# Optimization experiments

Hardware: AMD Instinct MI355X
Metric: run time of the kernel (lower is better)

## Reference

```python
import jax, jax.numpy as jnp
import numpy as np

B, D, H, W, N, R, K = 8, 192, 64, 64, 16, 6, 4
L = H * W
EPS = 1e-5


def setup_inputs() -> dict:
    key = jax.random.key(0)
    ks = jax.random.split(key, 6)
    return {
        "x": jax.random.normal(ks[0], (B, D, H, W), jnp.float32),
        "x_proj_weight": jax.random.normal(ks[1], (K, R + 2 * N, D), jnp.float32) * 0.05,
        "dt_projs_weight": jax.random.normal(ks[2], (K, D, R), jnp.float32) * 0.1,
        "dt_projs_bias": jax.random.normal(ks[3], (K, D), jnp.float32) * 0.1,
        "A_logs": jax.random.uniform(ks[4], (K * D, N), jnp.float32),  # A = -exp(A_logs) in (-e,-1)
        "Ds": jax.random.uniform(ks[5], (K * D,), jnp.float32),
        "norm_weight": jnp.ones((D,), jnp.float32),
        "norm_bias": jnp.zeros((D,), jnp.float32),
    }


def cross_scan(x):
    # x: [B,D,H,W] -> xs: [B,K=4,D,L]
    b, d, h, w = x.shape
    x0 = x.reshape(b, d, h * w)                      # row-major scan
    x1 = x.transpose(0, 1, 3, 2).reshape(b, d, h * w)  # column-major scan
    return jnp.stack([x0, x1, x0[..., ::-1], x1[..., ::-1]], axis=1)


def cross_merge(ys, h, w):
    # ys: [B,K=4,D,L] -> y: [B,D,L]
    b, k, d, l = ys.shape
    y01 = ys[:, 0] + ys[:, 2, :, ::-1]
    y23 = ys[:, 1] + ys[:, 3, :, ::-1]
    # undo the transpose of the column-major scan
    y23 = y23.reshape(b, d, w, h).transpose(0, 1, 3, 2).reshape(b, d, l)
    return y01 + y23


def selective_scan(u, dt, A, Bs, Cs, Dskip, dt_bias):
    # u, dt: [B,K,D,L]; A: [K,D,N]; Bs, Cs: [B,K,N,L]; Dskip, dt_bias: [K,D]
    dt = jax.nn.softplus(dt + dt_bias[None, :, :, None])
    dBu = dt * u
    # L-first for scan
    dt_l = dt.transpose(3, 0, 1, 2)    # [L,B,K,D]
    dBu_l = dBu.transpose(3, 0, 1, 2)  # [L,B,K,D]
    Bs_l = Bs.transpose(3, 0, 1, 2)    # [L,B,K,N]
    Cs_l = Cs.transpose(3, 0, 1, 2)    # [L,B,K,N]

    def step(h, inp):
        dt_t, dBu_t, B_t, C_t = inp
        dA = jnp.exp(dt_t[..., None] * A)                     # [B,K,D,N]
        h = h * dA + dBu_t[..., None] * B_t[:, :, None, :]    # [B,K,D,N]
        y = jnp.einsum('bkdn,bkn->bkd', h, C_t)
        return h, y

    h0 = jnp.zeros((u.shape[0], K, D, N), u.dtype)
    _, ys = jax.lax.scan(step, h0, (dt_l, dBu_l, Bs_l, Cs_l))
    ys = ys.transpose(1, 2, 3, 0)                             # [B,K,D,L]
    return ys + Dskip[None, :, :, None] * u


def reference(x, x_proj_weight, dt_projs_weight, dt_projs_bias, A_logs, Ds, norm_weight, norm_bias):
    b, d, h, w = x.shape
    l = h * w
    xs = cross_scan(x)                                        # [B,K,D,L]
    x_dbl = jnp.einsum('bkdl,kcd->bkcl', xs, x_proj_weight)   # [B,K,R+2N,L]
    dts, Bs, Cs = jnp.split(x_dbl, [R, R + N], axis=2)        # [B,K,R,L],[B,K,N,L],[B,K,N,L]
    dts = jnp.einsum('bkrl,kdr->bkdl', dts, dt_projs_weight)  # [B,K,D,L]
    A = -jnp.exp(A_logs).reshape(K, d, N)
    ys = selective_scan(xs, dts, A, Bs, Cs, Ds.reshape(K, d), dt_projs_bias)
    y = cross_merge(ys, h, w)                                 # [B,D,L]
    # out_norm (LayerNorm over channel dim, v0 path)
    y = y.transpose(0, 2, 1)                                  # [B,L,D]
    mu = jnp.mean(y, axis=-1, keepdims=True)
    var = jnp.mean(jnp.square(y - mu), axis=-1, keepdims=True)
    y = (y - mu) * jax.lax.rsqrt(var + EPS) * norm_weight + norm_bias
    return y.reshape(b, h, w, d).astype(x.dtype)
```

## Files before the change

kernel.cpp:

```cpp
#include <hip/hip_runtime.h>
#include <hip/hip_bf16.h>

#define LL 4096
#define DD 192
#define NN 16
#define NCH 128
#define LC  32

typedef float v2f __attribute__((ext_vector_type(2)));
typedef float f32x4 __attribute__((ext_vector_type(4)));
typedef short bf16x8 __attribute__((ext_vector_type(8)));

__device__ __forceinline__ v2f v2(float a, float b) { v2f r; r.x = a; r.y = b; return r; }
__device__ __forceinline__ float fexp2(float x) { return __builtin_amdgcn_exp2f(x); }

__global__ __launch_bounds__(192) void k_wprep(
    const float* __restrict__ Wp, __hip_bfloat16* __restrict__ Whi,
    __hip_bfloat16* __restrict__ Wlo)
{
  const int d = threadIdx.x;
  const int r = blockIdx.x;
  const int k = r / 48, cc = r % 48;
  float v = 0.f;
  if      (cc < 6)               v = Wp[((size_t)k * 38 + cc) * DD + d];
  else if (cc >= 8  && cc < 24)  v = Wp[((size_t)k * 38 + 6  + (cc - 8))  * DD + d];
  else if (cc >= 24 && cc < 40)  v = Wp[((size_t)k * 38 + 22 + (cc - 24)) * DD + d];
  const __hip_bfloat16 hi = __float2bfloat16(v);
  Whi[(size_t)r * DD + d] = hi;
  Wlo[(size_t)r * DD + d] = __float2bfloat16(v - __bfloat162float(hi));
}

__global__ __launch_bounds__(256) void k_an(
    const float* __restrict__ Alog, float* __restrict__ Ant)
{
  const int i = blockIdx.x * 256 + threadIdx.x;
  Ant[i] = -__expf(Alog[i]) * 1.4426950408889634f;
}

__global__ __launch_bounds__(256) void k_xt(
    const float* __restrict__ x, __hip_bfloat16* __restrict__ xh,
    __hip_bfloat16* __restrict__ xl)
{
  __shared__ float tile[64][65];
  const int b = blockIdx.z, d0 = blockIdx.y * 64, p0 = blockIdx.x * 64;
  const int tx = threadIdx.x & 63, ty = threadIdx.x >> 6;
#pragma unroll
  for (int r = ty; r < 64; r += 4)
    tile[r][tx] = x[((size_t)b * DD + d0 + r) * LL + p0 + tx];
  __syncthreads();
#pragma unroll
  for (int pr = ty; pr < 64; pr += 4) {
    const float vv = tile[tx][pr];
    const __hip_bfloat16 hi = __float2bfloat16(vv);
    const size_t idx = ((size_t)b * LL + p0 + pr) * DD + d0 + tx;
    xh[idx] = hi;
    xl[idx] = __float2bfloat16(vv - __bfloat162float(hi));
  }
}

__global__ __launch_bounds__(192) void k_mfproj(
    const __hip_bfloat16* __restrict__ xh, const __hip_bfloat16* __restrict__ xl,
    const __hip_bfloat16* __restrict__ Whi, const __hip_bfloat16* __restrict__ Wlo,
    float* __restrict__ dtr, float* __restrict__ Bsv, float* __restrict__ Csv)
{
  const int tid  = threadIdx.x;
  const int w    = tid >> 6;
  const int lane = tid & 63;
  const int n    = lane & 15;
  const int quad = lane >> 4;
  const int p0   = blockIdx.x * 16;
  const int b    = blockIdx.y;
  const int p    = p0 + n;

  const short* __restrict__ xhp = (const short*)xh + ((size_t)b * LL + p) * DD + quad * 8;
  const short* __restrict__ xlp = (const short*)xl + ((size_t)b * LL + p) * DD + quad * 8;
  const short* __restrict__ whp = (const short*)Whi + ((size_t)(w * 4) * 16 + n) * DD + quad * 8;
  const short* __restrict__ wlp = (const short*)Wlo + ((size_t)(w * 4) * 16 + n) * DD + quad * 8;

  f32x4 acc[4];
#pragma unroll
  for (int m = 0; m < 4; ++m) acc[m] = (f32x4){0.f, 0.f, 0.f, 0.f};

#pragma unroll
  for (int ks = 0; ks < 6; ++ks) {
    const bf16x8 bh = *(const bf16x8*)(xhp + ks * 32);
    const bf16x8 bl = *(const bf16x8*)(xlp + ks * 32);
#pragma unroll
    for (int m = 0; m < 4; ++m) {
      const bf16x8 ah = *(const bf16x8*)(whp + (size_t)m * 16 * DD + ks * 32);
      const bf16x8 al = *(const bf16x8*)(wlp + (size_t)m * 16 * DD + ks * 32);
      acc[m] = __builtin_amdgcn_mfma_f32_16x16x32_bf16(ah, bh, acc[m], 0, 0, 0);
      acc[m] = __builtin_amdgcn_mfma_f32_16x16x32_bf16(ah, bl, acc[m], 0, 0, 0);
      acc[m] = __builtin_amdgcn_mfma_f32_16x16x32_bf16(al, bh, acc[m], 0, 0, 0);
    }
  }

  const int sg = ((p & 63) << 6) | (p >> 6);
  int lsv[4] = { p, sg, LL - 1 - p, LL - 1 - sg };

#pragma unroll
  for (int m = 0; m < 4; ++m) {
    const int mt = w * 4 + m;
    const int k  = mt / 3;
    const int t  = mt - k * 3;
    const int cc0 = t * 16 + quad * 4;
    const size_t rowb = (size_t)(b * 4 + k) * LL + lsv[k];
    const float4 vv = make_float4(acc[m][0], acc[m][1], acc[m][2], acc[m][3]);
    if      (cc0 < 8)  *(float4*)(dtr + rowb * 8  + cc0)        = vv;
    else if (cc0 < 24) *(float4*)(Bsv + rowb * 16 + (cc0 - 8))  = vv;
    else if (cc0 < 40) *(float4*)(Csv + rowb * 16 + (cc0 - 24)) = vv;
  }
}

__device__ __forceinline__ int urow(int l, bool rev, bool trans) {
  const int rl = rev ? (LL - 1 - l) : l;
  return trans ? (((rl & 63) << 6) | (rl >> 6)) : rl;
}

__global__ __launch_bounds__(192, 6) void k_partial(
    const float* __restrict__ dtr, const float* __restrict__ Bsv,
    const __hip_bfloat16* __restrict__ xt, const float* __restrict__ Ant,
    const float* __restrict__ dtw, const float* __restrict__ dtb,
    __hip_bfloat16* __restrict__ Pv, __hip_bfloat16* __restrict__ qv)
{
  const int d  = threadIdx.x;
  const int bk = blockIdx.x;
  const int c  = blockIdx.y;
  const int k = bk & 3, b = bk >> 2;
  const int kd = k * DD + d;
  const bool rev = (k >= 2), trans = (k & 1);

  v2f An2[8];
  {
    const float4* __restrict__ at = (const float4*)(Ant + (size_t)kd * NN);
    const float4 t0 = at[0], t1 = at[1], t2 = at[2], t3 = at[3];
    An2[0]=v2(t0.x,t0.y); An2[1]=v2(t0.z,t0.w);
    An2[2]=v2(t1.x,t1.y); An2[3]=v2(t1.z,t1.w);
    An2[4]=v2(t2.x,t2.y); An2[5]=v2(t2.z,t2.w);
    An2[6]=v2(t3.x,t3.y); An2[7]=v2(t3.z,t3.w);
  }
  const float w0 = dtw[kd*6+0], w1 = dtw[kd*6+1], w2 = dtw[kd*6+2],
              w3 = dtw[kd*6+3], w4 = dtw[kd*6+4], w5 = dtw[kd*6+5];
  const float bias = dtb[kd];
  const __hip_bfloat16* __restrict__ ub = xt + (size_t)b * LL * DD + d;
  const float* __restrict__ dtrp = dtr + (size_t)bk * LL * 8;
  const float* __restrict__ Bp   = Bsv + (size_t)bk * LL * NN;

  float spsum = 0.f;
  v2f q2[8];
#pragma unroll
  for (int j = 0; j < 8; ++j) q2[j] = v2(0.f, 0.f);

  const int l0 = c * LC;
  float uc = __bfloat162float(ub[(size_t)urow(l0, rev, trans) * DD]);

#pragma unroll 2
  for (int i = 0; i < LC; ++i) {
    const int l = l0 + i;
    float un = 0.f;
    if (i + 1 < LC)
      un = __bfloat162float(ub[(size_t)urow(l + 1, rev, trans) * DD]);
    const float4 r0 = *(const float4*)(dtrp + (size_t)l * 8);
    const float2 r1 = *(const float2*)(dtrp + (size_t)l * 8 + 4);
    const float4 B0 = *(const float4*)(Bp + (size_t)l * NN);
    const float4 B1 = *(const float4*)(Bp + (size_t)l * NN + 4);
    const float4 B2 = *(const float4*)(Bp + (size_t)l * NN + 8);
    const float4 B3 = *(const float4*)(Bp + (size_t)l * NN + 12);
    float v = bias + r0.x*w0 + r0.y*w1 + r0.z*w2 + r0.w*w3 + r1.x*w4 + r1.y*w5;
    const float sp = (v > 20.f) ? v : __logf(1.f + __expf(v));
    const float dbu = sp * uc;
    spsum += sp;
    const v2f sp2  = v2(sp, sp);
    const v2f dbu2 = v2(dbu, dbu);
    const v2f Bv[8] = { v2(B0.x,B0.y), v2(B0.z,B0.w), v2(B1.x,B1.y), v2(B1.z,B1.w),
                        v2(B2.x,B2.y), v2(B2.z,B2.w), v2(B3.x,B3.y), v2(B3.z,B3.w) };
#pragma unroll
    for (int j = 0; j < 8; ++j) {
      const v2f a = sp2 * An2[j];
      v2f e; e.x = fexp2(a.x); e.y = fexp2(a.y);
      q2[j] = __builtin_elementwise_fma(q2[j], e, dbu2 * Bv[j]);
    }
    uc = un;
  }

  __hip_bfloat16* __restrict__ Pp = Pv + (((size_t)bk * NCH + c) * DD + d) * NN;
  __hip_bfloat16* __restrict__ qp = qv + (((size_t)bk * NCH + c) * DD + d) * NN;
#pragma unroll
  for (int j = 0; j < 8; ++j) {
    Pp[2*j]   = __float2bfloat16(fexp2(An2[j].x * spsum));
    Pp[2*j+1] = __float2bfloat16(fexp2(An2[j].y * spsum));
    qp[2*j]   = __float2bfloat16(q2[j].x);
    qp[2*j+1] = __float2bfloat16(q2[j].y);
  }
}

__global__ __launch_bounds__(256) void k_comb(
    __hip_bfloat16* __restrict__ Pv, const __hip_bfloat16* __restrict__ qv)
{
  const int idx = blockIdx.x * 256 + threadIdx.x;
  const int dn = idx % (DD * NN);
  const int bk = idx / (DD * NN);
  const size_t base = (size_t)bk * NCH * DD * NN + dn;
  float h = 0.f;
  for (int c = 0; c < NCH; ++c) {
    const size_t a = base + (size_t)c * DD * NN;
    const float Pc = __bfloat162float(Pv[a]);
    const float qc = __bfloat162float(qv[a]);
    Pv[a] = __float2bfloat16(h);
    h = fmaf(Pc, h, qc);
  }
}

__global__ __launch_bounds__(192, 6) void k_scanc(
    const float* __restrict__ dtr, const float* __restrict__ Bsv,
    const float* __restrict__ Csv, const __hip_bfloat16* __restrict__ xt,
    const float* __restrict__ Ant,
    const float* __restrict__ dtw, const float* __restrict__ dtb,
    const __hip_bfloat16* __restrict__ hin, __hip_bfloat16* __restrict__ ys)
{
  const int d  = threadIdx.x;
  const int bk = blockIdx.x;
  const int c  = blockIdx.y;
  const int k = bk & 3, b = bk >> 2;
  const int kd = k * DD + d;
  const bool rev = (k >= 2), trans = (k & 1);

  v2f An2[8];
  {
    const float4* __restrict__ at = (const float4*)(Ant + (size_t)kd * NN);
    const float4 t0 = at[0], t1 = at[1], t2 = at[2], t3 = at[3];
    An2[0]=v2(t0.x,t0.y); An2[1]=v2(t0.z,t0.w);
    An2[2]=v2(t1.x,t1.y); An2[3]=v2(t1.z,t1.w);
    An2[4]=v2(t2.x,t2.y); An2[5]=v2(t2.z,t2.w);
    An2[6]=v2(t3.x,t3.y); An2[7]=v2(t3.z,t3.w);
  }
  const float w0 = dtw[kd*6+0], w1 = dtw[kd*6+1], w2 = dtw[kd*6+2],
              w3 = dtw[kd*6+3], w4 = dtw[kd*6+4], w5 = dtw[kd*6+5];
  const float bias = dtb[kd];
  const __hip_bfloat16* __restrict__ ub = xt + (size_t)b * LL * DD + d;
  const float* __restrict__ dtrp = dtr + (size_t)bk * LL * 8;
  const float* __restrict__ Bp   = Bsv + (size_t)bk * LL * NN;
  const float* __restrict__ Cp   = Csv + (size_t)bk * LL * NN;
  __hip_bfloat16* __restrict__ yp = ys + (size_t)bk * LL * DD + d;

  v2f h2[8];
  const __hip_bfloat16* __restrict__ hp = hin + (((size_t)bk * NCH + c) * DD + d) * NN;
#pragma unroll
  for (int j = 0; j < 8; ++j)
    h2[j] = v2(__bfloat162float(hp[2*j]), __bfloat162float(hp[2*j+1]));

  const int l0 = c * LC;
  int rowc = urow(l0, rev, trans);
  float uc = __bfloat162float(ub[(size_t)rowc * DD]);

#pragma unroll 2
  for (int i = 0; i < LC; ++i) {
    const int l = l0 + i;
    int rown = 0; float un = 0.f;
    if (i + 1 < LC) {
      rown = urow(l + 1, rev, trans);
      un = __bfloat162float(ub[(size_t)rown * DD]);
    }
    const float4 r0 = *(const float4*)(dtrp + (size_t)l * 8);
    const float2 r1 = *(const float2*)(dtrp + (size_t)l * 8 + 4);
    const float4 B0 = *(const float4*)(Bp + (size_t)l * NN);
    const float4 B1 = *(const float4*)(Bp + (size_t)l * NN + 4);
    const float4 B2 = *(const float4*)(Bp + (size_t)l * NN + 8);
    const float4 B3 = *(const float4*)(Bp + (size_t)l * NN + 12);
    const float4 C0 = *(const float4*)(Cp + (size_t)l * NN);
    const float4 C1 = *(const float4*)(Cp + (size_t)l * NN + 4);
    const float4 C2 = *(const float4*)(Cp + (size_t)l * NN + 8);
    const float4 C3 = *(const float4*)(Cp + (size_t)l * NN + 12);
    float v = bias + r0.x*w0 + r0.y*w1 + r0.z*w2 + r0.w*w3 + r1.x*w4 + r1.y*w5;
    const float sp = (v > 20.f) ? v : __logf(1.f + __expf(v));
    const float dbu = sp * uc;
    const v2f sp2  = v2(sp, sp);
    const v2f dbu2 = v2(dbu, dbu);
    const v2f Bv[8] = { v2(B0.x,B0.y), v2(B0.z,B0.w), v2(B1.x,B1.y), v2(B1.z,B1.w),
                        v2(B2.x,B2.y), v2(B2.z,B2.w), v2(B3.x,B3.y), v2(B3.z,B3.w) };
    const v2f Cv[8] = { v2(C0.x,C0.y), v2(C0.z,C0.w), v2(C1.x,C1.y), v2(C1.z,C1.w),
                        v2(C2.x,C2.y), v2(C2.z,C2.w), v2(C3.x,C3.y), v2(C3.z,C3.w) };
    v2f ya = v2(0.f, 0.f), yb = v2(0.f, 0.f), yc = v2(0.f, 0.f), yd = v2(0.f, 0.f);
#pragma unroll
    for (int j = 0; j < 8; ++j) {
      const v2f a = sp2 * An2[j];
      v2f e; e.x = fexp2(a.x); e.y = fexp2(a.y);
      h2[j] = __builtin_elementwise_fma(h2[j], e, dbu2 * Bv[j]);
      v2f& yacc = (j < 2) ? ya : (j < 4) ? yb : (j < 6) ? yc : yd;
      yacc = __builtin_elementwise_fma(h2[j], Cv[j], yacc);
    }
    const v2f ysum = (ya + yb) + (yc + yd);
    yp[(size_t)rowc * DD] = __float2bfloat16(ysum.x + ysum.y);
    rowc = rown; uc = un;
  }
}

__global__ __launch_bounds__(64) void k_merge(
    const __hip_bfloat16* __restrict__ ys,
    const __hip_bfloat16* __restrict__ xh, const __hip_bfloat16* __restrict__ xl,
    const float* __restrict__ Ds, const float* __restrict__ nw,
    const float* __restrict__ nb, float* __restrict__ out)
{
  const int lane = threadIdx.x;
  const int b = blockIdx.y;
  const int q0 = blockIdx.x * 8;

  float Dsum[3], nwv[3], nbv[3];
#pragma unroll
  for (int i = 0; i < 3; ++i) {
    int d = lane + 64 * i;
    Dsum[i] = Ds[d] + Ds[DD + d] + Ds[2 * DD + d] + Ds[3 * DD + d];
    nwv[i] = nw[d];
    nbv[i] = nb[d];
  }
  const __hip_bfloat16* __restrict__ ysb = ys + (size_t)b * 4 * LL * DD;
  const __hip_bfloat16* __restrict__ xhb = xh + (size_t)b * LL * DD;
  const __hip_bfloat16* __restrict__ xlb = xl + (size_t)b * LL * DD;
  float* __restrict__ ob = out + (size_t)b * LL * DD;

  float v[8][3];
#pragma unroll
  for (int j = 0; j < 8; ++j) {
    const int pos = q0 + j;
#pragma unroll
    for (int i = 0; i < 3; ++i) {
      const int d = lane + 64 * i;
      const size_t idx = (size_t)pos * DD + d;
      float s = __bfloat162float(ysb[idx])
              + __bfloat162float(ysb[(size_t)LL * DD + idx])
              + __bfloat162float(ysb[(size_t)2 * LL * DD + idx])
              + __bfloat162float(ysb[(size_t)3 * LL * DD + idx]);
      const float xv = __bfloat162float(xhb[idx]) + __bfloat162float(xlb[idx]);
      v[j][i] = s + xv * Dsum[i];
    }
  }
#pragma unroll
  for (int j = 0; j < 8; ++j) {
    float s1 = v[j][0] + v[j][1] + v[j][2];
    float s2 = v[j][0]*v[j][0] + v[j][1]*v[j][1] + v[j][2]*v[j][2];
#pragma unroll
    for (int m = 1; m < 64; m <<= 1) {
      s1 += __shfl_xor(s1, m);
      s2 += __shfl_xor(s2, m);
    }
    const float mu  = s1 * (1.f / 192.f);
    const float var = s2 * (1.f / 192.f) - mu * mu;
    const float rs  = rsqrtf(var + 1e-5f);
    const int pos = q0 + j;
#pragma unroll
    for (int i = 0; i < 3; ++i) {
      ob[(size_t)pos * DD + lane + 64 * i] = (v[j][i] - mu) * rs * nwv[i] + nbv[i];
    }
  }
}

extern "C" void kernel_launch(void* const* d_in, const int* in_sizes, int n_in,
                              void* d_out, int out_size, void* d_ws, size_t ws_size,
                              hipStream_t stream)
{
  (void)in_sizes; (void)n_in; (void)out_size; (void)ws_size;
  const float* x    = (const float*)d_in[0];
  const float* Wp   = (const float*)d_in[1];
  const float* dtw  = (const float*)d_in[2];
  const float* dtb  = (const float*)d_in[3];
  const float* Alog = (const float*)d_in[4];
  const float* Ds   = (const float*)d_in[5];
  const float* nw   = (const float*)d_in[6];
  const float* nb   = (const float*)d_in[7];
  float* out = (float*)d_out;
  float* ws  = (float*)d_ws;

  float* dtrw = ws;
  float* Bsv  = ws + 1048576;
  float* Csv  = ws + 3145728;
  __hip_bfloat16* xh  = (__hip_bfloat16*)(ws + 5242880);
  __hip_bfloat16* ysv = (__hip_bfloat16*)(ws + 8388608);
  __hip_bfloat16* qv  = (__hip_bfloat16*)(ws + 11534336);
  __hip_bfloat16* Pv  = (__hip_bfloat16*)(ws + 20971520);
  __hip_bfloat16* Whi = (__hip_bfloat16*)(ws + 27262976);
  __hip_bfloat16* Wlo = (__hip_bfloat16*)(ws + 27281408);
  __hip_bfloat16* xlv = (__hip_bfloat16*)(ws + 27299840);
  float* Ant          = ws + 30445568;

  k_wprep  <<<192, 192, 0, stream>>>(Wp, Whi, Wlo);
  k_an     <<<48, 256, 0, stream>>>(Alog, Ant);
  k_xt     <<<dim3(64, 3, 8), 256, 0, stream>>>(x, xh, xlv);
  k_mfproj <<<dim3(256, 8), 192, 0, stream>>>(xh, xlv, Whi, Wlo, dtrw, Bsv, Csv);
  k_partial<<<dim3(32, NCH), DD, 0, stream>>>(dtrw, Bsv, xh, Ant, dtw, dtb, Pv, qv);
  k_comb   <<<384, 256, 0, stream>>>(Pv, qv);
  k_scanc  <<<dim3(32, NCH), DD, 0, stream>>>(dtrw, Bsv, Csv, xh, Ant, dtw, dtb, Pv, ysv);
  k_merge  <<<dim3(512, 8), 64, 0, stream>>>(ysv, xh, xlv, Ds, nw, nb, out);
}
```

Measured before the change: 331.9 us.

## Stage dt/B/C chunks into LDS via global_load_lds and batch u prefetch

In the partial-state and chunked-scan kernels, each wave now copies the chunk's dt-projection, B and C rows into its own LDS region with direct global-to-LDS loads. Inner loops then read these per-timestep values from shared memory instead of issuing the same broadcast global loads from every thread. The u inputs are prefetched eight timesteps at a time in registers as raw bf16 bits, replacing the single-step lookahead. Occupancy hints drop from 6 to 4 waves, which trades latency hiding for more registers and LDS per block.

```diff
diff --git a/kernel.cpp b/kernel.cpp
--- a/kernel.cpp
+++ b/kernel.cpp
@@ -13,6 +13,10 @@
 
 __device__ __forceinline__ v2f v2(float a, float b) { v2f r; r.x = a; r.y = b; return r; }
 __device__ __forceinline__ float fexp2(float x) { return __builtin_amdgcn_exp2f(x); }
+
+#define GLDS16(gp, lp) __builtin_amdgcn_global_load_lds(                      \
+    (const __attribute__((address_space(1))) void*)(gp),                      \
+    (__attribute__((address_space(3))) void*)(lp), 16, 0, 0)
 
 __global__ __launch_bounds__(192) void k_wprep(
     const float* __restrict__ Wp, __hip_bfloat16* __restrict__ Whi,
@@ -117,18 +121,31 @@
   return trans ? (((rl & 63) << 6) | (rl >> 6)) : rl;
 }
 
-__global__ __launch_bounds__(192, 6) void k_partial(
+__global__ __launch_bounds__(192, 4) void k_partial(
     const float* __restrict__ dtr, const float* __restrict__ Bsv,
     const __hip_bfloat16* __restrict__ xt, const float* __restrict__ Ant,
     const float* __restrict__ dtw, const float* __restrict__ dtb,
     __hip_bfloat16* __restrict__ Pv, __hip_bfloat16* __restrict__ qv)
 {
+  __shared__ __align__(16) float smem[3][LC * 24];
   const int d  = threadIdx.x;
+  const int wav = d >> 6, lane = d & 63;
   const int bk = blockIdx.x;
   const int c  = blockIdx.y;
   const int k = bk & 3, b = bk >> 2;
   const int kd = k * DD + d;
   const bool rev = (k >= 2), trans = (k & 1);
+  const int l0 = c * LC;
+
+  float* sdtr = smem[wav];
+  float* sB   = smem[wav] + LC * 8;
+  {
+    const float* gdtr = dtr + ((size_t)bk * LL + l0) * 8;
+    const float* gB   = Bsv + ((size_t)bk * LL + l0) * NN;
+    GLDS16(gdtr + lane * 4, sdtr);
+    GLDS16(gB + lane * 4, sB);
+    GLDS16(gB + 256 + lane * 4, sB + 256);
+  }
 
   v2f An2[8];
   {
@@ -142,45 +159,53 @@
   const float w0 = dtw[kd*6+0], w1 = dtw[kd*6+1], w2 = dtw[kd*6+2],
               w3 = dtw[kd*6+3], w4 = dtw[kd*6+4], w5 = dtw[kd*6+5];
   const float bias = dtb[kd];
-  const __hip_bfloat16* __restrict__ ub = xt + (size_t)b * LL * DD + d;
-  const float* __restrict__ dtrp = dtr + (size_t)bk * LL * 8;
-  const float* __restrict__ Bp   = Bsv + (size_t)bk * LL * NN;
+  const ushort* __restrict__ up = (const ushort*)xt + (size_t)b * LL * DD + d;
+
+  uint ucur[8], unext[8] = {0,0,0,0,0,0,0,0};
+#pragma unroll
+  for (int i = 0; i < 8; ++i)
+    ucur[i] = up[(size_t)urow(l0 + i, rev, trans) * DD];
+
+  asm volatile("s_waitcnt vmcnt(0)" ::: "memory");
 
   float spsum = 0.f;
   v2f q2[8];
 #pragma unroll
   for (int j = 0; j < 8; ++j) q2[j] = v2(0.f, 0.f);
 
-  const int l0 = c * LC;
-  float uc = __bfloat162float(ub[(size_t)urow(l0, rev, trans) * DD]);
-
-#pragma unroll 2
-  for (int i = 0; i < LC; ++i) {
-    const int l = l0 + i;
-    float un = 0.f;
-    if (i + 1 < LC)
-      un = __bfloat162float(ub[(size_t)urow(l + 1, rev, trans) * DD]);
-    const float4 r0 = *(const float4*)(dtrp + (size_t)l * 8);
-    const float2 r1 = *(const float2*)(dtrp + (size_t)l * 8 + 4);
-    const float4 B0 = *(const float4*)(Bp + (size_t)l * NN);
-    const float4 B1 = *(const float4*)(Bp + (size_t)l * NN + 4);
-    const float4 B2 = *(const float4*)(Bp + (size_t)l * NN + 8);
-    const float4 B3 = *(const float4*)(Bp + (size_t)l * NN + 12);
-    float v = bias + r0.x*w0 + r0.y*w1 + r0.z*w2 + r0.w*w3 + r1.x*w4 + r1.y*w5;
-    const float sp = (v > 20.f) ? v : __logf(1.f + __expf(v));
-    const float dbu = sp * uc;
-    spsum += sp;
-    const v2f sp2  = v2(sp, sp);
-    const v2f dbu2 = v2(dbu, dbu);
-    const v2f Bv[8] = { v2(B0.x,B0.y), v2(B0.z,B0.w), v2(B1.x,B1.y), v2(B1.z,B1.w),
-                        v2(B2.x,B2.y), v2(B2.z,B2.w), v2(B3.x,B3.y), v2(B3.z,B3.w) };
-#pragma unroll
-    for (int j = 0; j < 8; ++j) {
-      const v2f a = sp2 * An2[j];
-      v2f e; e.x = fexp2(a.x); e.y = fexp2(a.y);
-      q2[j] = __builtin_elementwise_fma(q2[j], e, dbu2 * Bv[j]);
-    }
-    uc = un;
+  for (int g = 0; g < 4; ++g) {
+    if (g < 3) {
+#pragma unroll
+      for (int i = 0; i < 8; ++i)
+        unext[i] = up[(size_t)urow(l0 + 8 * g + 8 + i, rev, trans) * DD];
+    }
+#pragma unroll
+    for (int ii = 0; ii < 8; ++ii) {
+      const int i = 8 * g + ii;
+      const float uc = __uint_as_float(ucur[ii] << 16);
+      const float4 r0 = *(const float4*)(sdtr + i * 8);
+      const float2 r1 = *(const float2*)(sdtr + i * 8 + 4);
+      const float4 B0 = *(const float4*)(sB + i * 16);
+      const float4 B1 = *(const float4*)(sB + i * 16 + 4);
+      const float4 B2 = *(const float4*)(sB + i * 16 + 8);
+      const float4 B3 = *(const float4*)(sB + i * 16 + 12);
+      float v = bias + r0.x*w0 + r0.y*w1 + r0.z*w2 + r0.w*w3 + r1.x*w4 + r1.y*w5;
+      const float sp = (v > 20.f) ? v : __logf(1.f + __expf(v));
+      const float dbu = sp * uc;
+      spsum += sp;
+      const v2f sp2  = v2(sp, sp);
+      const v2f dbu2 = v2(dbu, dbu);
+      const v2f Bv[8] = { v2(B0.x,B0.y), v2(B0.z,B0.w), v2(B1.x,B1.y), v2(B1.z,B1.w),
+                          v2(B2.x,B2.y), v2(B2.z,B2.w), v2(B3.x,B3.y), v2(B3.z,B3.w) };
+#pragma unroll
+      for (int j = 0; j < 8; ++j) {
+        const v2f a = sp2 * An2[j];
+        v2f e; e.x = fexp2(a.x); e.y = fexp2(a.y);
+        q2[j] = __builtin_elementwise_fma(q2[j], e, dbu2 * Bv[j]);
+      }
+    }
+#pragma unroll
+    for (int i = 0; i < 8; ++i) ucur[i] = unext[i];
   }
 
   __hip_bfloat16* __restrict__ Pp = Pv + (((size_t)bk * NCH + c) * DD + d) * NN;
@@ -211,19 +236,36 @@
   }
 }
 
-__global__ __launch_bounds__(192, 6) void k_scanc(
+__global__ __launch_bounds__(192, 4) void k_scanc(
     const float* __restrict__ dtr, const float* __restrict__ Bsv,
     const float* __restrict__ Csv, const __hip_bfloat16* __restrict__ xt,
     const float* __restrict__ Ant,
     const float* __restrict__ dtw, const float* __restrict__ dtb,
     const __hip_bfloat16* __restrict__ hin, __hip_bfloat16* __restrict__ ys)
 {
+  __shared__ __align__(16) float smem[3][LC * 40];
   const int d  = threadIdx.x;
+  const int wav = d >> 6, lane = d & 63;
   const int bk = blockIdx.x;
   const int c  = blockIdx.y;
   const int k = bk & 3, b = bk >> 2;
   const int kd = k * DD + d;
   const bool rev = (k >= 2), trans = (k & 1);
+  const int l0 = c * LC;
+
+  float* sdtr = smem[wav];
+  float* sB   = smem[wav] + LC * 8;
+  float* sC   = smem[wav] + LC * 24;
+  {
+    const float* gdtr = dtr + ((size_t)bk * LL + l0) * 8;
+    const float* gB   = Bsv + ((size_t)bk * LL + l0) * NN;
+    const float* gC   = Csv + ((size_t)bk * LL + l0) * NN;
+    GLDS16(gdtr + lane * 4, sdtr);
+    GLDS16(gB + lane * 4, sB);
+    GLDS16(gB + 256 + lane * 4, sB + 256);
+    GLDS16(gC + lane * 4, sC);
+    GLDS16(gC + 256 + lane * 4, sC + 256);
+  }
 
   v2f An2[8];
   {
@@ -237,10 +279,7 @@
   const float w0 = dtw[kd*6+0], w1 = dtw[kd*6+1], w2 = dtw[kd*6+2],
               w3 = dtw[kd*6+3], w4 = dtw[kd*6+4], w5 = dtw[kd*6+5];
   const float bias = dtb[kd];
-  const __hip_bfloat16* __restrict__ ub = xt + (size_t)b * LL * DD + d;
-  const float* __restrict__ dtrp = dtr + (size_t)bk * LL * 8;
-  const float* __restrict__ Bp   = Bsv + (size_t)bk * LL * NN;
-  const float* __restrict__ Cp   = Csv + (size_t)bk * LL * NN;
+  const ushort* __restrict__ up = (const ushort*)xt + (size_t)b * LL * DD + d;
   __hip_bfloat16* __restrict__ yp = ys + (size_t)bk * LL * DD + d;
 
   v2f h2[8];
@@ -249,49 +288,58 @@
   for (int j = 0; j < 8; ++j)
     h2[j] = v2(__bfloat162float(hp[2*j]), __bfloat162float(hp[2*j+1]));
 
-  const int l0 = c * LC;
-  int rowc = urow(l0, rev, trans);
-  float uc = __bfloat162float(ub[(size_t)rowc * DD]);
-
-#pragma unroll 2
-  for (int i = 0; i < LC; ++i) {
-    const int l = l0 + i;
-    int rown = 0; float un = 0.f;
-    if (i + 1 < LC) {
-      rown = urow(l + 1, rev, trans);
-      un = __bfloat162float(ub[(size_t)rown * DD]);
-    }
-    const float4 r0 = *(const float4*)(dtrp + (size_t)l * 8);
-    const float2 r1 = *(const float2*)(dtrp + (size_t)l * 8 + 4);
-    const float4 B0 = *(const float4*)(Bp + (size_t)l * NN);
-    const float4 B1 = *(const float4*)(Bp + (size_t)l * NN + 4);
-    const float4 B2 = *(const float4*)(Bp + (size_t)l * NN + 8);
-    const float4 B3 = *(const float4*)(Bp + (size_t)l * NN + 12);
-    const float4 C0 = *(const float4*)(Cp + (size_t)l * NN);
-    const float4 C1 = *(const float4*)(Cp + (size_t)l * NN + 4);
-    const float4 C2 = *(const float4*)(Cp + (size_t)l * NN + 8);
-    const float4 C3 = *(const float4*)(Cp + (size_t)l * NN + 12);
-    float v = bias + r0.x*w0 + r0.y*w1 + r0.z*w2 + r0.w*w3 + r1.x*w4 + r1.y*w5;
-    const float sp = (v > 20.f) ? v : __logf(1.f + __expf(v));
-    const float dbu = sp * uc;
-    const v2f sp2  = v2(sp, sp);
-    const v2f dbu2 = v2(dbu, dbu);
-    const v2f Bv[8] = { v2(B0.x,B0.y), v2(B0.z,B0.w), v2(B1.x,B1.y), v2(B1.z,B1.w),
-                        v2(B2.x,B2.y), v2(B2.z,B2.w), v2(B3.x,B3.y), v2(B3.z,B3.w) };
-    const v2f Cv[8] = { v2(C0.x,C0.y), v2(C0.z,C0.w), v2(C1.x,C1.y), v2(C1.z,C1.w),
-                        v2(C2.x,C2.y), v2(C2.z,C2.w), v2(C3.x,C3.y), v2(C3.z,C3.w) };
-    v2f ya = v2(0.f, 0.f), yb = v2(0.f, 0.f), yc = v2(0.f, 0.f), yd = v2(0.f, 0.f);
-#pragma unroll
-    for (int j = 0; j < 8; ++j) {
-      const v2f a = sp2 * An2[j];
-      v2f e; e.x = fexp2(a.x); e.y = fexp2(a.y);
-      h2[j] = __builtin_elementwise_fma(h2[j], e, dbu2 * Bv[j]);
-      v2f& yacc = (j < 2) ? ya : (j < 4) ? yb : (j < 6) ? yc : yd;
-      yacc = __builtin_elementwise_fma(h2[j], Cv[j], yacc);
-    }
-    const v2f ysum = (ya + yb) + (yc + yd);
-    yp[(size_t)rowc * DD] = __float2bfloat16(ysum.x + ysum.y);
-    rowc = rown; uc = un;
+  uint ucur[8], unext[8] = {0,0,0,0,0,0,0,0};
+#pragma unroll
+  for (int i = 0; i < 8; ++i)
+    ucur[i] = up[(size_t)urow(l0 + i, rev, trans) * DD];
+
+  asm volatile("s_waitcnt vmcnt(0)" ::: "memory");
+
+  for (int g = 0; g < 4; ++g) {
+    if (g < 3) {
+#pragma unroll
+      for (int i = 0; i < 8; ++i)
+        unext[i] = up[(size_t)urow(l0 + 8 * g + 8 + i, rev, trans) * DD];
+    }
+#pragma unroll
+    for (int ii = 0; ii < 8; ++ii) {
+      const int i = 8 * g + ii;
+      const int l = l0 + i;
+      const int rowc = urow(l, rev, trans);
+      const float uc = __uint_as_float(ucur[ii] << 16);
+      const float4 r0 = *(const float4*)(sdtr + i * 8);
+      const float2 r1 = *(const float2*)(sdtr + i * 8 + 4);
+      const float4 B0 = *(const float4*)(sB + i * 16);
+      const float4 B1 = *(const float4*)(sB + i * 16 + 4);
+      const float4 B2 = *(const float4*)(sB + i * 16 + 8);
+      const float4 B3 = *(const float4*)(sB + i * 16 + 12);
+      const float4 C0 = *(const float4*)(sC + i * 16);
+      const float4 C1 = *(const float4*)(sC + i * 16 + 4);
+      const float4 C2 = *(const float4*)(sC + i * 16 + 8);
+      const float4 C3 = *(const float4*)(sC + i * 16 + 12);
+      float v = bias + r0.x*w0 + r0.y*w1 + r0.z*w2 + r0.w*w3 + r1.x*w4 + r1.y*w5;
+      const float sp = (v > 20.f) ? v : __logf(1.f + __expf(v));
+      const float dbu = sp * uc;
+      const v2f sp2  = v2(sp, sp);
+      const v2f dbu2 = v2(dbu, dbu);
+      const v2f Bv[8] = { v2(B0.x,B0.y), v2(B0.z,B0.w), v2(B1.x,B1.y), v2(B1.z,B1.w),
+                          v2(B2.x,B2.y), v2(B2.z,B2.w), v2(B3.x,B3.y), v2(B3.z,B3.w) };
+      const v2f Cv[8] = { v2(C0.x,C0.y), v2(C0.z,C0.w), v2(C1.x,C1.y), v2(C1.z,C1.w),
+                          v2(C2.x,C2.y), v2(C2.z,C2.w), v2(C3.x,C3.y), v2(C3.z,C3.w) };
+      v2f ya = v2(0.f, 0.f), yb = v2(0.f, 0.f), yc = v2(0.f, 0.f), yd = v2(0.f, 0.f);
+#pragma unroll
+      for (int j = 0; j < 8; ++j) {
+        const v2f a = sp2 * An2[j];
+        v2f e; e.x = fexp2(a.x); e.y = fexp2(a.y);
+        h2[j] = __builtin_elementwise_fma(h2[j], e, dbu2 * Bv[j]);
+        v2f& yacc = (j < 2) ? ya : (j < 4) ? yb : (j < 6) ? yc : yd;
+        yacc = __builtin_elementwise_fma(h2[j], Cv[j], yacc);
+      }
+      const v2f ysum = (ya + yb) + (yc + yd);
+      yp[(size_t)rowc * DD] = __float2bfloat16(ysum.x + ysum.y);
+    }
+#pragma unroll
+    for (int i = 0; i < 8; ++i) ucur[i] = unext[i];
   }
 }
 
```

Result: no change. 326.2 us (-1.7%).
